# Performance work log

Measured on AMD Instinct MI355X. Metric: run time of the kernel, lower is better.

## Reference

```python
import jax, jax.numpy as jnp
import numpy as np

N_STEPS = 128
DT = 0.001
TAU_M = 10.0 * DT            # NeuroTorch LIFLayer default tau_m = 10*dt
ALPHA = float(np.exp(-DT / TAU_M))
THRESHOLD = 1.0
GAMMA = 100.0                # surrogate-gradient sharpness

@jax.custom_vjp
def spike_fn(v):
    # Heaviside spike with sigmoid surrogate gradient (HeavisideSigmoidApprox)
    return (v >= THRESHOLD).astype(v.dtype)

def _spike_fwd(v):
    return spike_fn(v), v

def _spike_bwd(v, g):
    s = jax.nn.sigmoid(GAMMA * (v - THRESHOLD))
    return (g * GAMMA * s * (1.0 - s),)

spike_fn.defvjp(_spike_fwd, _spike_bwd)

def setup_inputs() -> dict:
    key = jax.random.key(0)
    B, N = 256, 2048
    x = jax.random.normal(key, (B, N), dtype=jnp.float32)
    W = jnp.eye(N, dtype=jnp.float32)  # default forward_weights = eye(n_units)
    return {"x": x, "W": W}

def reference(x, W):
    B, N = x.shape
    # ConstantValuesTransform repeats x over all n_steps, so the input current
    # I = x @ W is identical every step; hoist it out of the scan.
    I = x @ W  # [B, N]
    V0 = jnp.zeros((B, N), dtype=x.dtype)
    Z0 = jnp.zeros((B, N), dtype=x.dtype)

    def step(carry, _):
        V, Z = carry
        # reset via previous spikes (detached in original: Z.detach())
        V_next = (ALPHA * V + I) * (1.0 - jax.lax.stop_gradient(Z))
        Z_next = spike_fn(V_next)
        return (V_next, Z_next), Z_next

    _, spikes = jax.lax.scan(step, (V0, Z0), None, length=N_STEPS)  # [T, B, N]
    return jnp.transpose(spikes, (1, 0, 2))  # [B, T, N] like torch.stack(dim=1)
```

## Files before the change

kernel.cpp:

```cpp
#include <hip/hip_runtime.h>
#include <cstddef>

#define Mdim 256
#define Ndim 2048
#define Kdim 2048
#define Tsteps 128


typedef float v4f __attribute__((ext_vector_type(4)));

__global__ __launch_bounds__(256) void scan_w_kernel(
    const float* __restrict__ W, unsigned char* __restrict__ flags)
{
    const int c = blockIdx.x;
    const int g = blockIdx.y;
    const int tid = threadIdx.x;

    __shared__ int wmask[4];

    const int coff = (tid & 31) * 4;
    const int rbase = tid >> 5;

    unsigned mask = 0;
#pragma unroll
    for (int it = 0; it < 16; ++it) {
        const int r = it * 8 + rbase;
        const float4 v = *(const float4*)&W[(size_t)(g * 128 + r) * Ndim + c * 128 + coff];
        const bool nz = (v.x != 0.0f) | (v.y != 0.0f) | (v.z != 0.0f) | (v.w != 0.0f);
        mask |= (nz ? 1u : 0u) << (it >> 1);
    }
#pragma unroll
    for (int off = 32; off; off >>= 1) mask |= __shfl_down(mask, off);
    if ((tid & 63) == 0) wmask[tid >> 6] = (int)mask;
    __syncthreads();
    if (tid == 0) {
        const int m = wmask[0] | wmask[1] | wmask[2] | wmask[3];
        flags[c * 16 + g] = (unsigned char)m;
    }
}

__global__ __launch_bounds__(256) void lif_fused_kernel(
    const float* __restrict__ x, const float* __restrict__ W,
    const unsigned* __restrict__ flags, float* __restrict__ out)
{
    __shared__ float xs[Kdim];

    const int tid = threadIdx.x;
    const int b = blockIdx.x >> 1;
    const int n = ((blockIdx.x & 1) << 10) + tid * 4;
    const int c = n >> 7;

    {
        const float* xp = x + (size_t)b * Kdim;
        *(float4*)&xs[tid * 4]        = *(const float4*)&xp[tid * 4];
        *(float4*)&xs[1024 + tid * 4] = *(const float4*)&xp[1024 + tid * 4];
    }
    __syncthreads();

    float f0 = 0.0f, f1 = 0.0f, f2 = 0.0f, f3 = 0.0f;
#pragma unroll
    for (int w = 0; w < 4; ++w) {
        unsigned word = flags[c * 4 + w];
        while (word) {
            const int bit = __builtin_ctz(word);
            word &= word - 1;
            const int k0 = (w * 32 + bit) * 16;
            const float* wp = W + (size_t)k0 * Ndim + n;
#pragma unroll
            for (int kk = 0; kk < 16; ++kk) {
                const float xv = xs[k0 + kk];
                const float4 wv = *(const float4*)(wp + (size_t)kk * Ndim);
                f0 = fmaf(xv, wv.x, f0);
                f1 = fmaf(xv, wv.y, f1);
                f2 = fmaf(xv, wv.z, f2);
                f3 = fmaf(xv, wv.w, f3);
            }
        }
    }
    const float Iv[4] = {f0, f1, f2, f3};

    const float ALPHA = (float)0.9048374180359595;

    float V[4] = {0.0f, 0.0f, 0.0f, 0.0f};
    float Z[4] = {0.0f, 0.0f, 0.0f, 0.0f};

    float* op = out + (size_t)b * Tsteps * Ndim + n;
#pragma unroll 4
    for (int t = 0; t < Tsteps; ++t) {
#pragma unroll
        for (int j = 0; j < 4; ++j) {
            float v = __fmul_rn(ALPHA, V[j]);
            v = __fadd_rn(v, Iv[j]);
            v = __fmul_rn(v, __fsub_rn(1.0f, Z[j]));
            V[j] = v;
            Z[j] = (v >= 1.0f) ? 1.0f : 0.0f;
        }
        v4f s = {Z[0], Z[1], Z[2], Z[3]};
        __builtin_nontemporal_store(s, (v4f*)&op[(size_t)t * Ndim]);
    }
}

extern "C" void kernel_launch(void* const* d_in, const int* in_sizes, int n_in,
                              void* d_out, int out_size, void* d_ws, size_t ws_size,
                              hipStream_t stream) {
    const float* x = (const float*)d_in[0];
    const float* W = (const float*)d_in[1];
    float* out = (float*)d_out;

    unsigned char* flags = (unsigned char*)d_ws;

    scan_w_kernel<<<dim3(16, 16), 256, 0, stream>>>(W, flags);

    const int sim_blocks = Mdim * Ndim / 1024;
    lif_fused_kernel<<<dim3(sim_blocks), 256, 0, stream>>>(
        x, W, (const unsigned*)flags, out);
}
```

Measured before the change: 298.2 us.

## Split fused LIF kernel into block-sparse GEMM plus separate simulation kernel

Moves the block-sparse x@W product into its own kernel, where each thread computes 8 batch rows for one column and reuses every W element across those rows. Previously each of the 512 simulation blocks re-read W independently. The simulation kernel now just loads the precomputed current from workspace, runs the LIF recurrence with unroll 8, and uses launch bounds of 2 blocks. This adds an extra kernel launch and a round trip of I through global memory, and the new GEMM reads x with strided, uncoalesced scalar loads.

```diff
diff --git a/kernel.cpp b/kernel.cpp
--- a/kernel.cpp
+++ b/kernel.cpp
@@ -6,8 +6,8 @@
 #define Kdim 2048
 #define Tsteps 128
 
+typedef float v4f __attribute__((ext_vector_type(4)));
 
-typedef float v4f __attribute__((ext_vector_type(4)));
 
 __global__ __launch_bounds__(256) void scan_w_kernel(
     const float* __restrict__ W, unsigned char* __restrict__ flags)
@@ -39,25 +39,20 @@
     }
 }
 
-__global__ __launch_bounds__(256) void lif_fused_kernel(
+__global__ __launch_bounds__(256) void gemm_flagged_kernel(
     const float* __restrict__ x, const float* __restrict__ W,
-    const unsigned* __restrict__ flags, float* __restrict__ out)
+    const unsigned* __restrict__ flags, float* __restrict__ I)
 {
-    __shared__ float xs[Kdim];
+    const int c  = blockIdx.x;
+    const int mb = blockIdx.y;
+    const int tid = threadIdx.x;
+    const int n  = c * 128 + (tid & 127);
+    const int b0 = mb * 16 + (tid >> 7) * 8;
 
-    const int tid = threadIdx.x;
-    const int b = blockIdx.x >> 1;
-    const int n = ((blockIdx.x & 1) << 10) + tid * 4;
-    const int c = n >> 7;
+    float f[8];
+#pragma unroll
+    for (int i = 0; i < 8; ++i) f[i] = 0.0f;
 
-    {
-        const float* xp = x + (size_t)b * Kdim;
-        *(float4*)&xs[tid * 4]        = *(const float4*)&xp[tid * 4];
-        *(float4*)&xs[1024 + tid * 4] = *(const float4*)&xp[1024 + tid * 4];
-    }
-    __syncthreads();
-
-    float f0 = 0.0f, f1 = 0.0f, f2 = 0.0f, f3 = 0.0f;
 #pragma unroll
     for (int w = 0; w < 4; ++w) {
         unsigned word = flags[c * 4 + w];
@@ -66,18 +61,30 @@
             word &= word - 1;
             const int k0 = (w * 32 + bit) * 16;
             const float* wp = W + (size_t)k0 * Ndim + n;
+            const float* xp = x + k0;
 #pragma unroll
             for (int kk = 0; kk < 16; ++kk) {
-                const float xv = xs[k0 + kk];
-                const float4 wv = *(const float4*)(wp + (size_t)kk * Ndim);
-                f0 = fmaf(xv, wv.x, f0);
-                f1 = fmaf(xv, wv.y, f1);
-                f2 = fmaf(xv, wv.z, f2);
-                f3 = fmaf(xv, wv.w, f3);
+                const float wv = wp[(size_t)kk * Ndim];
+#pragma unroll
+                for (int i = 0; i < 8; ++i)
+                    f[i] = fmaf(xp[(size_t)(b0 + i) * Kdim + kk], wv, f[i]);
             }
         }
     }
-    const float Iv[4] = {f0, f1, f2, f3};
+#pragma unroll
+    for (int i = 0; i < 8; ++i)
+        I[(size_t)(b0 + i) * Ndim + n] = f[i];
+}
+
+__global__ __launch_bounds__(256, 2) void lif_sim_kernel(
+    const float* __restrict__ I, float* __restrict__ out)
+{
+    const int tid = threadIdx.x;
+    const int b = blockIdx.x >> 1;
+    const int n = ((blockIdx.x & 1) << 10) + tid * 4;
+
+    const float4 I4 = *(const float4*)&I[(size_t)b * Ndim + n];
+    const float Iv[4] = {I4.x, I4.y, I4.z, I4.w};
 
     const float ALPHA = (float)0.9048374180359595;
 
@@ -85,7 +92,7 @@
     float Z[4] = {0.0f, 0.0f, 0.0f, 0.0f};
 
     float* op = out + (size_t)b * Tsteps * Ndim + n;
-#pragma unroll 4
+#pragma unroll 8
     for (int t = 0; t < Tsteps; ++t) {
 #pragma unroll
         for (int j = 0; j < 4; ++j) {
@@ -96,7 +103,7 @@
             Z[j] = (v >= 1.0f) ? 1.0f : 0.0f;
         }
         v4f s = {Z[0], Z[1], Z[2], Z[3]};
-        __builtin_nontemporal_store(s, (v4f*)&op[(size_t)t * Ndim]);
+        __builtin_nontemporal_store(s, (v4f*)(op + (size_t)t * Ndim));
     }
 }
 
@@ -108,10 +115,13 @@
     float* out = (float*)d_out;
 
     unsigned char* flags = (unsigned char*)d_ws;
+    float* I = (float*)((char*)d_ws + 4096);
 
     scan_w_kernel<<<dim3(16, 16), 256, 0, stream>>>(W, flags);
 
+    gemm_flagged_kernel<<<dim3(16, 16), 256, 0, stream>>>(
+        x, W, (const unsigned*)flags, I);
+
     const int sim_blocks = Mdim * Ndim / 1024;
-    lif_fused_kernel<<<dim3(sim_blocks), 256, 0, stream>>>(
-        x, W, (const unsigned*)flags, out);
+    lif_sim_kernel<<<dim3(sim_blocks), 256, 0, stream>>>(I, out);
 }
```

New measurement: 297.6 us. No clear change (-0.2%).
